# Kernel tuning notes

Hardware: AMD Instinct MI355X
Metric: run time of the kernel (lower is better)

The kernel has to match this reference:

```python
import jax, jax.numpy as jnp
import numpy as np

N_NODES = 50000
N_EDGES = 1600000
IN_DIM = 128
HID = 128
OUT_DIM = 3
NEG_SLOPE = 0.01  # LeakyReLU default


def _glorot(key, shape):
    fan_in, fan_out = shape[0], shape[1]
    lim = jnp.sqrt(6.0 / (fan_in + fan_out))
    return jax.random.uniform(key, shape, jnp.float32, -lim, lim)


def setup_inputs() -> dict:
    key = jax.random.key(0)
    ks = jax.random.split(key, 12)
    feature = jax.random.normal(ks[0], (N_NODES, IN_DIM), jnp.float32)
    edge_index = jax.random.randint(ks[1], (2, N_EDGES), 0, N_NODES, jnp.int64)
    edge_type = jax.random.randint(ks[2], (N_EDGES,), 0, 2, jnp.int64)
    return {
        'feature': feature,
        'edge_index': edge_index,
        'edge_type': edge_type,
        'W_in': _glorot(ks[3], (IN_DIM, HID)),
        'b_in': jnp.zeros((HID,), jnp.float32),
        'W1_l': _glorot(ks[4], (HID, HID)),  # SAGEConv lin_l (aggregated neighbors, has bias)
        'b1_l': jnp.zeros((HID,), jnp.float32),
        'W1_r': _glorot(ks[5], (HID, HID)),  # SAGEConv lin_r (root/self, no bias)
        'W2_l': _glorot(ks[6], (HID, HID)),
        'b2_l': jnp.zeros((HID,), jnp.float32),
        'W2_r': _glorot(ks[7], (HID, HID)),
        'W_out': _glorot(ks[8], (HID, OUT_DIM)),
        'b_out': jnp.zeros((OUT_DIM,), jnp.float32),
    }


def _sage_conv(x, src, dst, W_l, b_l, W_r):
    # PyG SAGEConv with mean aggregation: out = lin_l(mean_{j in N(i)} x_j) + lin_r(x_i)
    msg = x[src]                                              # [E, HID] gather
    summed = jax.ops.segment_sum(msg, dst, num_segments=x.shape[0])
    cnt = jax.ops.segment_sum(jnp.ones((src.shape[0],), x.dtype), dst,
                              num_segments=x.shape[0])
    agg = summed / jnp.maximum(cnt, 1.0)[:, None]             # isolated nodes -> 0
    return agg @ W_l + b_l + x @ W_r


def reference(feature, edge_index, edge_type, W_in, b_in, W1_l, b1_l, W1_r,
              W2_l, b2_l, W2_r, W_out, b_out):
    src, dst = edge_index[0], edge_index[1]
    x = jax.nn.leaky_relu(feature.astype(jnp.float32) @ W_in + b_in, NEG_SLOPE)
    x = _sage_conv(x, src, dst, W1_l, b1_l, W1_r)
    # dropout inactive in eval mode
    x = _sage_conv(x, src, dst, W2_l, b2_l, W2_r)
    return x @ W_out + b_out
```

## Files before the change

### kernel.cpp

```cpp
#include <hip/hip_runtime.h>
#include <hip/hip_bf16.h>

#define NEG_SLOPE 0.01f
#define BNODES 256
#define NBE 256

typedef __attribute__((ext_vector_type(8))) short short8;
typedef __attribute__((ext_vector_type(4))) float f32x4;
typedef __attribute__((ext_vector_type(2))) float f32x2;

__device__ __forceinline__ unsigned short f2bf(float f) {
  unsigned int u = __float_as_uint(f);
  u = (u + 0x7fffu + ((u >> 16) & 1u)) >> 16;
  return (unsigned short)u;
}
__device__ __forceinline__ float bf2f(unsigned short b) {
  return __uint_as_float(((unsigned)b) << 16);
}

#if defined(__has_builtin)
#if __has_builtin(__builtin_amdgcn_cvt_pk_f32_fp8) && __has_builtin(__builtin_amdgcn_cvt_pk_fp8_f32)
#define HAS_FP8_CVT 1
#endif
#endif
#ifndef HAS_FP8_CVT
#define HAS_FP8_CVT 0
#endif

__device__ __forceinline__ float dec1(unsigned b) {
  unsigned s = (b & 0x80u) << 24;
  unsigned em = b & 0x7fu;
  float v = (em < 8) ? (float)em * 0.001953125f
          : __uint_as_float((((em >> 3) + 120u) << 23) | ((em & 7u) << 20));
  return __uint_as_float(s ^ __float_as_uint(v));
}

__device__ __forceinline__ unsigned enc1(float f) {
  unsigned u = __float_as_uint(f);
  unsigned s = (u >> 24) & 0x80u;
  float a = fabsf(f);
  a = fminf(a, 480.f);
  unsigned code;
  if (a < 0.015625f) {
    code = (unsigned)__float2int_rn(a * 512.f);
  } else {
    unsigned ua = __float_as_uint(a);
    unsigned r = ua + 0x7ffffu + ((ua >> 20) & 1u);
    code = (((r >> 23) - 120u) << 3) | ((r >> 20) & 7u);
    if (code > 0x7fu) code = 0x7fu;
  }
  return s | code;
}

template<bool HI>
__device__ __forceinline__ f32x2 fp8pair(unsigned int w) {
#if HAS_FP8_CVT
  return __builtin_amdgcn_cvt_pk_f32_fp8((int)w, HI);
#else
  unsigned sh = HI ? 16u : 0u;
  f32x2 r;
  r[0] = dec1((w >> sh) & 0xffu);
  r[1] = dec1((w >> (sh + 8)) & 0xffu);
  return r;
#endif
}

template<bool HI>
__device__ __forceinline__ unsigned fp8pack(float a, float b, unsigned old) {
#if HAS_FP8_CVT
  return (unsigned)__builtin_amdgcn_cvt_pk_fp8_f32(a, b, (int)old, HI);
#else
  unsigned code = enc1(a) | (enc1(b) << 8);
  return HI ? ((old & 0x0000ffffu) | (code << 16)) : ((old & 0xffff0000u) | code);
#endif
}

__global__ __launch_bounds__(256) void k_prep_hist(
    const float* __restrict__ w0, const float* __restrict__ w1,
    const float* __restrict__ w2, const float* __restrict__ w3,
    const float* __restrict__ w4, unsigned short* __restrict__ wout,
    const int* __restrict__ dst, int* __restrict__ hist, int E)
{
  if (blockIdx.x < 5) {
    const float* srcs[5] = {w0, w1, w2, w3, w4};
    const float* s = srcs[blockIdx.x];
    unsigned short* o = wout + (size_t)blockIdx.x * 16384;
    for (int i = threadIdx.x; i < 16384; i += 256) {
      int c = i >> 7, k = i & 127;
      o[i] = f2bf(s[(size_t)k * 128 + c]);
    }
    return;
  }
  __shared__ int lh[256];
  const int bb = blockIdx.x - 5;
  int t = threadIdx.x;
  lh[t] = 0;
  __syncthreads();
  int chunk = (E + NBE - 1) / NBE;
  int s = bb * chunk;
  int e = min(E, s + chunk);
  for (int i = s + t; i < e; i += 256)
    atomicAdd(&lh[dst[i] >> 8], 1);
  __syncthreads();
  hist[bb * 256 + t] = lh[t];
}

__global__ __launch_bounds__(256) void k_scan(const int* __restrict__ hist,
    int* __restrict__ offs, int NB)
{
  __shared__ int tot[256];
  int t = threadIdx.x;
  int run = 0;
  #pragma unroll 8
  for (int b = 0; b < NBE; ++b) run += hist[b * 256 + t];
  tot[t] = run;
  __syncthreads();
  int val = run;
  for (int o = 1; o < 256; o <<= 1) {
    int x = (t >= o) ? tot[t - o] : 0;
    __syncthreads();
    val += x; tot[t] = val;
    __syncthreads();
  }
  int acc = val - run;
  #pragma unroll 8
  for (int b = 0; b < NBE; ++b) {
    offs[b * 256 + t] = acc;
    acc += hist[b * 256 + t];
  }
  (void)NB;
}

__global__ __launch_bounds__(256) void k_scatter(const int* __restrict__ src,
    const int* __restrict__ dst, const int* __restrict__ offs,
    unsigned int* __restrict__ recs, int E)
{
  __shared__ int lcnt[256];
  __shared__ int loff[256];
  int t = threadIdx.x;
  lcnt[t] = 0;
  loff[t] = offs[blockIdx.x * 256 + t];
  __syncthreads();
  int chunk = (E + NBE - 1) / NBE;
  int s = blockIdx.x * chunk;
  int e = min(E, s + chunk);
  for (int i = s + t; i < e; i += 256) {
    int d = dst[i];
    int b = d >> 8;
    int r = atomicAdd(&lcnt[b], 1);
    recs[loff[b] + r] = ((unsigned int)(d & 255) << 16) | (unsigned int)src[i];
  }
}

__device__ __forceinline__ void csr_body(int b, int* lcnt, int* lpos,
    const unsigned int* __restrict__ recs, const int* __restrict__ offs,
    int* __restrict__ adj, int* __restrict__ offs2, int* __restrict__ cnt,
    int N, int NB, int E)
{
  const int t  = threadIdx.x;
  const int bs = offs[b];
  const int be = (b + 1 < NB) ? offs[b + 1] : E;
  lcnt[t] = 0;
  __syncthreads();
  for (int i = bs + t; i < be; i += 256)
    atomicAdd(&lcnt[recs[i] >> 16], 1);
  __syncthreads();
  int v = lcnt[t];
  lpos[t] = v;
  __syncthreads();
  int val = v;
  for (int o = 1; o < 256; o <<= 1) {
    int x = (t >= o) ? lpos[t - o] : 0;
    __syncthreads();
    val += x; lpos[t] = val;
    __syncthreads();
  }
  int excl = val - v;
  int node = b * BNODES + t;
  if (node < N) { cnt[node] = v; offs2[node] = bs + excl; }
  lcnt[t] = excl;
  __syncthreads();
  for (int i = bs + t; i < be; i += 256) {
    unsigned int r = recs[i];
    int ld = r >> 16;
    int p = atomicAdd(&lcnt[ld], 1);
    adj[bs + p] = (int)(r & 0xffffu);
  }
}

template<bool ACT, bool HAS2, bool A1F32, bool EMIT8, bool OUTPROJ>
__device__ __forceinline__ void mgemm_body(int b, char* wlds,
    const void* __restrict__ A1v, const unsigned short* __restrict__ Wt1,
    const float* __restrict__ bias,
    const unsigned short* __restrict__ A2b, const unsigned short* __restrict__ Wt2,
    unsigned short* __restrict__ Cb, unsigned int* __restrict__ C8,
    const float* __restrict__ Wo, const float* __restrict__ bo,
    float* __restrict__ outp, int nrows)
{
  const int t    = threadIdx.x;
  const int wave = t >> 6;
  const int lane = t & 63;
  const int lr   = lane & 15;
  const int lg   = lane >> 4;
  const int r0   = b * 64 + wave * 16;
  int arow = r0 + lr; if (arow >= nrows) arow = nrows - 1;

  short8 a1[4], a2[4];
  #pragma unroll
  for (int ks = 0; ks < 4; ++ks) {
    const int k0 = ks * 32 + lg * 8;
    if (A1F32) {
      const float* A = (const float*)A1v;
      float4 f0 = *(const float4*)(A + (size_t)arow * 128 + k0);
      float4 f1 = *(const float4*)(A + (size_t)arow * 128 + k0 + 4);
      a1[ks][0] = (short)f2bf(f0.x); a1[ks][1] = (short)f2bf(f0.y);
      a1[ks][2] = (short)f2bf(f0.z); a1[ks][3] = (short)f2bf(f0.w);
      a1[ks][4] = (short)f2bf(f1.x); a1[ks][5] = (short)f2bf(f1.y);
      a1[ks][6] = (short)f2bf(f1.z); a1[ks][7] = (short)f2bf(f1.w);
    } else {
      a1[ks] = *(const short8*)((const unsigned short*)A1v + (size_t)arow * 128 + k0);
    }
  }
  if (HAS2) {
    #pragma unroll
    for (int ks = 0; ks < 4; ++ks) {
      const int k0 = ks * 32 + lg * 8;
      a2[ks] = *(const short8*)(A2b + (size_t)arow * 128 + k0);
    }
  }

  f32x4 acc[8];
  #pragma unroll
  for (int i = 0; i < 8; ++i) acc[i] = (f32x4){0.f, 0.f, 0.f, 0.f};

  #pragma unroll
  for (int i = 0; i < 8; ++i) {
    int o = (i * 256 + t) * 16;
    uint4 v = *(const uint4*)((const char*)Wt1 + o);
    int row = o >> 8, w = o & 255;
    *(uint4*)(wlds + row * 256 + (w ^ ((row & 7) << 4))) = v;
  }
  __syncthreads();
  #pragma unroll
  for (int ks = 0; ks < 4; ++ks) {
    #pragma unroll
    for (int cb = 0; cb < 8; ++cb) {
      int r = cb * 16 + lr;
      int wb = ks * 64 + lg * 16;
      short8 bv = *(const short8*)(wlds + r * 256 + (wb ^ ((r & 7) << 4)));
      acc[cb] = __builtin_amdgcn_mfma_f32_16x16x32_bf16(a1[ks], bv, acc[cb], 0, 0, 0);
    }
  }

  if (HAS2) {
    __syncthreads();
    #pragma unroll
    for (int i = 0; i < 8; ++i) {
      int o = (i * 256 + t) * 16;
      uint4 v = *(const uint4*)((const char*)Wt2 + o);
      int row = o >> 8, w = o & 255;
      *(uint4*)(wlds + row * 256 + (w ^ ((row & 7) << 4))) = v;
    }
    __syncthreads();
    #pragma unroll
    for (int ks = 0; ks < 4; ++ks) {
      #pragma unroll
      for (int cb = 0; cb < 8; ++cb) {
        int r = cb * 16 + lr;
        int wb = ks * 64 + lg * 16;
        short8 bv = *(const short8*)(wlds + r * 256 + (wb ^ ((r & 7) << 4)));
        acc[cb] = __builtin_amdgcn_mfma_f32_16x16x32_bf16(a2[ks], bv, acc[cb], 0, 0, 0);
      }
    }
  }

  __syncthreads();
  #pragma unroll
  for (int cb = 0; cb < 8; ++cb) {
    const int col = cb * 16 + lr;
    const float bcol = bias[col];
    #pragma unroll
    for (int reg = 0; reg < 4; ++reg) {
      const int lrow = wave * 16 + lg * 4 + reg;
      float o = acc[cb][reg] + bcol;
      if (ACT) o = o > 0.f ? o : o * NEG_SLOPE;
      *(unsigned short*)(wlds + lrow * 256 + col * 2) = f2bf(o);
    }
  }
  __syncthreads();

  if (!OUTPROJ) {
    #pragma unroll
    for (int i = 0; i < 4; ++i) {
      int idx = i * 256 + t;
      int row = idx >> 4, w = idx & 15;
      int r = b * 64 + row;
      if (r < nrows)
        *(uint4*)((char*)Cb + (size_t)r * 256 + w * 16) = *(const uint4*)(wlds + row * 256 + w * 16);
    }
    if (EMIT8) {
      #pragma unroll
      for (int i = 0; i < 4; ++i) {
        int idx = i * 256 + t;
        int row = idx >> 4, seg = idx & 15;
        int r = b * 64 + row;
        if (r < nrows) {
          const unsigned short* p = (const unsigned short*)(wlds + row * 256 + seg * 16);
          unsigned w0 = 0, w1 = 0;
          w0 = fp8pack<false>(bf2f(p[0]), bf2f(p[1]), w0);
          w0 = fp8pack<true >(bf2f(p[2]), bf2f(p[3]), w0);
          w1 = fp8pack<false>(bf2f(p[4]), bf2f(p[5]), w1);
          w1 = fp8pack<true >(bf2f(p[6]), bf2f(p[7]), w1);
          *(uint2*)(C8 + (size_t)r * 32 + seg * 2) = make_uint2(w0, w1);
        }
      }
    }
  } else {
    const int row = t >> 2, q = t & 3;
    const int r = b * 64 + row;
    float o0 = 0.f, o1 = 0.f, o2 = 0.f;
    const unsigned short* p = (const unsigned short*)(wlds + row * 256 + q * 64);
    #pragma unroll
    for (int i = 0; i < 32; ++i) {
      float x = bf2f(p[i]);
      const float* wr = Wo + (q * 32 + i) * 3;
      o0 += x * wr[0]; o1 += x * wr[1]; o2 += x * wr[2];
    }
    o0 += __shfl_xor(o0, 1, 64); o0 += __shfl_xor(o0, 2, 64);
    o1 += __shfl_xor(o1, 1, 64); o1 += __shfl_xor(o1, 2, 64);
    o2 += __shfl_xor(o2, 1, 64); o2 += __shfl_xor(o2, 2, 64);
    if (q == 0 && r < nrows) {
      outp[(size_t)r * 3 + 0] = o0 + bo[0];
      outp[(size_t)r * 3 + 1] = o1 + bo[1];
      outp[(size_t)r * 3 + 2] = o2 + bo[2];
    }
  }
}

__global__ __launch_bounds__(256) void k_csr_mgemm0(
    const unsigned int* __restrict__ recs, const int* __restrict__ offs,
    int* __restrict__ adj, int* __restrict__ offs2, int* __restrict__ cnt,
    const float* __restrict__ feature, const unsigned short* __restrict__ WtIn,
    const float* __restrict__ b_in,
    unsigned short* __restrict__ xbs, unsigned int* __restrict__ x8,
    int N, int NB, int E)
{
  __shared__ char wlds[32768];
  if ((int)blockIdx.x < NB) {
    int* li = (int*)wlds;
    csr_body(blockIdx.x, li, li + 256, recs, offs, adj, offs2, cnt, N, NB, E);
    return;
  }
  mgemm_body<true, false, true, true, false>(blockIdx.x - NB, wlds,
      feature, WtIn, b_in, nullptr, nullptr, xbs, x8, nullptr, nullptr, nullptr, N);
}

template<bool EMIT8, bool OUTPROJ>
__global__ __launch_bounds__(256) void k_mgemm(
    const unsigned short* __restrict__ A1b, const unsigned short* __restrict__ Wt1,
    const float* __restrict__ bias,
    const unsigned short* __restrict__ A2b, const unsigned short* __restrict__ Wt2,
    unsigned short* __restrict__ Cb, unsigned int* __restrict__ C8,
    const float* __restrict__ Wo, const float* __restrict__ bo,
    float* __restrict__ outp, int nrows)
{
  __shared__ char wlds[32768];
  mgemm_body<false, true, false, EMIT8, OUTPROJ>(blockIdx.x, wlds,
      A1b, Wt1, bias, A2b, Wt2, Cb, C8, Wo, bo, outp, nrows);
}

__global__ __launch_bounds__(256) void k_agg(const unsigned int* __restrict__ x8,
    const int* __restrict__ adj, const int* __restrict__ offs2,
    const int* __restrict__ cnt, unsigned int* __restrict__ aggb, int n, int nJ)
{
  const int Q   = (nJ + 7) >> 3;
  const int x   = blockIdx.x & 7;
  const int t2  = blockIdx.x >> 3;
  const int jj  = t2 % Q;
  const int sub = t2 / Q;
  const int j   = x + (jj << 3);
  if (j >= nJ) return;
  int node = j * 64 + sub * 4 + (threadIdx.x >> 6);
  if (node >= n) return;

  const int lane = threadIdx.x & 63;
  const int l = lane & 15;
  const int q = lane >> 4;
  const int c = cnt[node];
  const int* __restrict__ a = adj + offs2[node];

  f32x2 acc[4];
  #pragma unroll
  for (int jv = 0; jv < 4; ++jv) acc[jv] = (f32x2){0.f, 0.f};

  if (c > 0) {
    const int cm1 = c - 1;
    for (int e0 = 0; e0 < c; e0 += 32) {
      int idx[8];
      #pragma unroll
      for (int s = 0; s < 8; ++s)
        idx[s] = a[min(e0 + s * 4 + q, cm1)];
      uint2 v[8];
      #pragma unroll
      for (int s = 0; s < 8; ++s)
        v[s] = *(const uint2*)(x8 + (size_t)idx[s] * 32 + l * 2);
      #pragma unroll
      for (int s = 0; s < 8; ++s) {
        float m = (e0 + s * 4 + q < c) ? 1.f : 0.f;
        f32x2 mm = (f32x2){m, m};
        acc[0] += mm * fp8pair<false>(v[s].x);
        acc[1] += mm * fp8pair<true >(v[s].x);
        acc[2] += mm * fp8pair<false>(v[s].y);
        acc[3] += mm * fp8pair<true >(v[s].y);
      }
    }
    #pragma unroll
    for (int jv = 0; jv < 4; ++jv) {
      float a0 = acc[jv][0], a1 = acc[jv][1];
      a0 += __shfl_xor(a0, 16, 64);
      a0 += __shfl_xor(a0, 32, 64);
      a1 += __shfl_xor(a1, 16, 64);
      a1 += __shfl_xor(a1, 32, 64);
      acc[jv][0] = a0; acc[jv][1] = a1;
    }
  }

  if (q == 0) {
    float sc = (c > 0) ? 1.f / (float)c : 0.f;
    uint4 w;
    w.x = (unsigned)f2bf(acc[0][0] * sc) | ((unsigned)f2bf(acc[0][1] * sc) << 16);
    w.y = (unsigned)f2bf(acc[1][0] * sc) | ((unsigned)f2bf(acc[1][1] * sc) << 16);
    w.z = (unsigned)f2bf(acc[2][0] * sc) | ((unsigned)f2bf(acc[2][1] * sc) << 16);
    w.w = (unsigned)f2bf(acc[3][0] * sc) | ((unsigned)f2bf(acc[3][1] * sc) << 16);
    *(uint4*)(aggb + (size_t)node * 64 + l * 4) = w;
  }
}

extern "C" void kernel_launch(void* const* d_in, const int* in_sizes, int n_in,
                              void* d_out, int out_size, void* d_ws, size_t ws_size,
                              hipStream_t stream)
{
  const float* feature = (const float*)d_in[0];
  const int*   ei      = (const int*)d_in[1];
  const float* W_in = (const float*)d_in[3];
  const float* b_in = (const float*)d_in[4];
  const float* W1l  = (const float*)d_in[5];
  const float* b1l  = (const float*)d_in[6];
  const float* W1r  = (const float*)d_in[7];
  const float* W2l  = (const float*)d_in[8];
  const float* b2l  = (const float*)d_in[9];
  const float* W2r  = (const float*)d_in[10];
  const float* Wo   = (const float*)d_in[11];
  const float* bo   = (const float*)d_in[12];
  float* out = (float*)d_out;

  const int N = in_sizes[0] / 128;
  const int E = in_sizes[1] / 2;
  const int NB = (N + BNODES - 1) / BNODES;
  const int* src = ei;
  const int* dst = ei + E;

  char* ws = (char*)d_ws;
  size_t off = 0;
  auto alloc = [&](size_t bytes) {
    char* p = ws + off;
    off = (off + bytes + 255) & ~(size_t)255;
    return p;
  };
  unsigned int* xb    = (unsigned int*)alloc((size_t)N * 64 * 4);
  unsigned int* yb    = (unsigned int*)alloc((size_t)N * 64 * 4);
  unsigned int* agb   = (unsigned int*)alloc((size_t)N * 64 * 4);
  unsigned int* x8    = (unsigned int*)alloc((size_t)N * 32 * 4);
  unsigned int* y8    = (unsigned int*)alloc((size_t)N * 32 * 4);
  unsigned int* recs  = (unsigned int*)alloc((size_t)E * 4);
  int*          adj   = (int*)alloc((size_t)E * 4);
  int*          hist  = (int*)alloc((size_t)256 * NBE * 4);
  int*          offs  = (int*)alloc((size_t)256 * NBE * 4);
  int*          offs2 = (int*)alloc((size_t)N * 4);
  int*          cnt   = (int*)alloc((size_t)N * 4);
  unsigned short* wtb = (unsigned short*)alloc((size_t)5 * 16384 * 2);
  (void)ws_size; (void)n_in; (void)out_size;

  unsigned short* WtIn = wtb;
  unsigned short* Wt1l = wtb + 16384;
  unsigned short* Wt1r = wtb + 2 * 16384;
  unsigned short* Wt2l = wtb + 3 * 16384;
  unsigned short* Wt2r = wtb + 4 * 16384;

  unsigned short* xbs  = (unsigned short*)xb;
  unsigned short* ybs  = (unsigned short*)yb;
  unsigned short* agbs = (unsigned short*)agb;

  dim3 blk(256);
  int gGemm = (N + 63) / 64;
  int Q     = (gGemm + 7) / 8;
  int gAgg  = 8 * Q * 16;

  k_prep_hist<<<5 + NBE, blk, 0, stream>>>(W_in, W1l, W1r, W2l, W2r, wtb,
                                           dst, hist, E);
  k_scan<<<1, blk, 0, stream>>>(hist, offs, NB);
  k_scatter<<<NBE, blk, 0, stream>>>(src, dst, offs, recs, E);
  k_csr_mgemm0<<<NB + gGemm, blk, 0, stream>>>(recs, offs, adj, offs2, cnt,
      feature, WtIn, b_in, xbs, x8, N, NB, E);
  k_agg<<<gAgg, blk, 0, stream>>>(x8, adj, offs2, cnt, agb, N, gGemm);
  k_mgemm<true, false><<<gGemm, blk, 0, stream>>>(
      agbs, Wt1l, b1l, xbs, Wt1r, ybs, y8, nullptr, nullptr, nullptr, N);
  k_agg<<<gAgg, blk, 0, stream>>>(y8, adj, offs2, cnt, agb, N, gGemm);
  k_mgemm<false, true><<<gGemm, blk, 0, stream>>>(
      agbs, Wt2l, b2l, ybs, Wt2r, nullptr, nullptr, Wo, bo, out, N);
}
```

Measured before the change: 172.1 us.

## Fuse all pipeline stages into one cooperative persistent kernel with grid syncs

Replaces the eight separate kernel launches (prep/hist, scan, scatter, CSR+input GEMM, two aggregations, two GEMMs) with a single cooperative persistent kernel. The grid is sized from occupancy and uses grid.sync between stages, with blocks looping over virtual block IDs. The aim is to remove launch gaps and inter-kernel tail effects. In exchange, the grid is capped at 2048 blocks, the scan runs on one block while the rest wait, and the launch bounds hint of 4 blocks per unit may constrain registers. The old multi-launch path remains as a fallback if the cooperative launch fails.

Result: slower. 608.6 us (+253.7%).

```diff
diff --git a/kernel.cpp b/kernel.cpp
--- a/kernel.cpp
+++ b/kernel.cpp
@@ -1,5 +1,8 @@
 #include <hip/hip_runtime.h>
 #include <hip/hip_bf16.h>
+#include <hip/hip_cooperative_groups.h>
+
+namespace cg = cooperative_groups;
 
 #define NEG_SLOPE 0.01f
 #define BNODES 256
@@ -75,24 +78,23 @@
 #endif
 }
 
-__global__ __launch_bounds__(256) void k_prep_hist(
-    const float* __restrict__ w0, const float* __restrict__ w1,
-    const float* __restrict__ w2, const float* __restrict__ w3,
-    const float* __restrict__ w4, unsigned short* __restrict__ wout,
+
+__device__ __forceinline__ void prep_body(int vb,
+    const float* w0, const float* w1, const float* w2, const float* w3,
+    const float* w4, unsigned short* wout)
+{
+  const float* srcs[5] = {w0, w1, w2, w3, w4};
+  const float* s = srcs[vb];
+  unsigned short* o = wout + (size_t)vb * 16384;
+  for (int i = threadIdx.x; i < 16384; i += 256) {
+    int c = i >> 7, k = i & 127;
+    o[i] = f2bf(s[(size_t)k * 128 + c]);
+  }
+}
+
+__device__ __forceinline__ void hist_body(int bb, int* lh,
     const int* __restrict__ dst, int* __restrict__ hist, int E)
 {
-  if (blockIdx.x < 5) {
-    const float* srcs[5] = {w0, w1, w2, w3, w4};
-    const float* s = srcs[blockIdx.x];
-    unsigned short* o = wout + (size_t)blockIdx.x * 16384;
-    for (int i = threadIdx.x; i < 16384; i += 256) {
-      int c = i >> 7, k = i & 127;
-      o[i] = f2bf(s[(size_t)k * 128 + c]);
-    }
-    return;
-  }
-  __shared__ int lh[256];
-  const int bb = blockIdx.x - 5;
   int t = threadIdx.x;
   lh[t] = 0;
   __syncthreads();
@@ -105,10 +107,9 @@
   hist[bb * 256 + t] = lh[t];
 }
 
-__global__ __launch_bounds__(256) void k_scan(const int* __restrict__ hist,
-    int* __restrict__ offs, int NB)
-{
-  __shared__ int tot[256];
+__device__ __forceinline__ void scan_body(int* tot,
+    const int* __restrict__ hist, int* __restrict__ offs)
+{
   int t = threadIdx.x;
   int run = 0;
   #pragma unroll 8
@@ -128,21 +129,18 @@
     offs[b * 256 + t] = acc;
     acc += hist[b * 256 + t];
   }
-  (void)NB;
-}
-
-__global__ __launch_bounds__(256) void k_scatter(const int* __restrict__ src,
-    const int* __restrict__ dst, const int* __restrict__ offs,
-    unsigned int* __restrict__ recs, int E)
-{
-  __shared__ int lcnt[256];
-  __shared__ int loff[256];
+}
+
+__device__ __forceinline__ void scatter_body(int bb, int* lcnt, int* loff,
+    const int* __restrict__ src, const int* __restrict__ dst,
+    const int* __restrict__ offs, unsigned int* __restrict__ recs, int E)
+{
   int t = threadIdx.x;
   lcnt[t] = 0;
-  loff[t] = offs[blockIdx.x * 256 + t];
+  loff[t] = offs[bb * 256 + t];
   __syncthreads();
   int chunk = (E + NBE - 1) / NBE;
-  int s = blockIdx.x * chunk;
+  int s = bb * chunk;
   int e = min(E, s + chunk);
   for (int i = s + t; i < e; i += 256) {
     int d = dst[i];
@@ -337,45 +335,13 @@
   }
 }
 
-__global__ __launch_bounds__(256) void k_csr_mgemm0(
-    const unsigned int* __restrict__ recs, const int* __restrict__ offs,
-    int* __restrict__ adj, int* __restrict__ offs2, int* __restrict__ cnt,
-    const float* __restrict__ feature, const unsigned short* __restrict__ WtIn,
-    const float* __restrict__ b_in,
-    unsigned short* __restrict__ xbs, unsigned int* __restrict__ x8,
-    int N, int NB, int E)
-{
-  __shared__ char wlds[32768];
-  if ((int)blockIdx.x < NB) {
-    int* li = (int*)wlds;
-    csr_body(blockIdx.x, li, li + 256, recs, offs, adj, offs2, cnt, N, NB, E);
-    return;
-  }
-  mgemm_body<true, false, true, true, false>(blockIdx.x - NB, wlds,
-      feature, WtIn, b_in, nullptr, nullptr, xbs, x8, nullptr, nullptr, nullptr, N);
-}
-
-template<bool EMIT8, bool OUTPROJ>
-__global__ __launch_bounds__(256) void k_mgemm(
-    const unsigned short* __restrict__ A1b, const unsigned short* __restrict__ Wt1,
-    const float* __restrict__ bias,
-    const unsigned short* __restrict__ A2b, const unsigned short* __restrict__ Wt2,
-    unsigned short* __restrict__ Cb, unsigned int* __restrict__ C8,
-    const float* __restrict__ Wo, const float* __restrict__ bo,
-    float* __restrict__ outp, int nrows)
-{
-  __shared__ char wlds[32768];
-  mgemm_body<false, true, false, EMIT8, OUTPROJ>(blockIdx.x, wlds,
-      A1b, Wt1, bias, A2b, Wt2, Cb, C8, Wo, bo, outp, nrows);
-}
-
-__global__ __launch_bounds__(256) void k_agg(const unsigned int* __restrict__ x8,
+__device__ __forceinline__ void agg_body(int vb, const unsigned int* __restrict__ x8,
     const int* __restrict__ adj, const int* __restrict__ offs2,
     const int* __restrict__ cnt, unsigned int* __restrict__ aggb, int n, int nJ)
 {
   const int Q   = (nJ + 7) >> 3;
-  const int x   = blockIdx.x & 7;
-  const int t2  = blockIdx.x >> 3;
+  const int x   = vb & 7;
+  const int t2  = vb >> 3;
   const int jj  = t2 % Q;
   const int sub = t2 / Q;
   const int j   = x + (jj << 3);
@@ -436,6 +402,147 @@
   }
 }
 
+
+struct MegaArgs {
+  const float* feature;
+  const int* src; const int* dst;
+  const float *W_in, *b_in, *W1l, *b1l, *W1r, *W2l, *b2l, *W2r, *Wo, *bo;
+  unsigned short* wtb;
+  unsigned short* xbs; unsigned int* x8;
+  unsigned short* ybs; unsigned int* y8;
+  unsigned short* agbs; unsigned int* agb;
+  unsigned int* recs; int* adj; int* hist; int* offs; int* offs2; int* cnt;
+  float* out;
+  int N, E, NB, gGemm, gAgg;
+};
+
+__global__ __launch_bounds__(256, 4) void k_mega(MegaArgs a)
+{
+  __shared__ char smem[32768];
+  cg::grid_group grid = cg::this_grid();
+  const int G   = (int)gridDim.x;
+  const int bid = (int)blockIdx.x;
+
+  for (int vb = bid; vb < 5 + NBE; vb += G) {
+    if (vb < 5) prep_body(vb, a.W_in, a.W1l, a.W1r, a.W2l, a.W2r, a.wtb);
+    else        hist_body(vb - 5, (int*)smem, a.dst, a.hist, a.E);
+    __syncthreads();
+  }
+  grid.sync();
+
+  if (bid == 0) scan_body((int*)smem, a.hist, a.offs);
+  grid.sync();
+
+  for (int vb = bid; vb < NBE; vb += G) {
+    int* li = (int*)smem;
+    scatter_body(vb, li, li + 256, a.src, a.dst, a.offs, a.recs, a.E);
+    __syncthreads();
+  }
+  grid.sync();
+
+  for (int vb = bid; vb < a.NB + a.gGemm; vb += G) {
+    if (vb < a.NB) {
+      int* li = (int*)smem;
+      csr_body(vb, li, li + 256, a.recs, a.offs, a.adj, a.offs2, a.cnt, a.N, a.NB, a.E);
+    } else {
+      mgemm_body<true, false, true, true, false>(vb - a.NB, smem,
+          a.feature, a.wtb, a.b_in, nullptr, nullptr,
+          a.xbs, a.x8, nullptr, nullptr, nullptr, a.N);
+    }
+    __syncthreads();
+  }
+  grid.sync();
+
+  for (int vb = bid; vb < a.gAgg; vb += G)
+    agg_body(vb, a.x8, a.adj, a.offs2, a.cnt, a.agb, a.N, a.gGemm);
+  grid.sync();
+
+  for (int vb = bid; vb < a.gGemm; vb += G) {
+    mgemm_body<false, true, false, true, false>(vb, smem,
+        a.agbs, a.wtb + 16384, a.b1l, a.xbs, a.wtb + 2 * 16384,
+        a.ybs, a.y8, nullptr, nullptr, nullptr, a.N);
+    __syncthreads();
+  }
+  grid.sync();
+
+  for (int vb = bid; vb < a.gAgg; vb += G)
+    agg_body(vb, a.y8, a.adj, a.offs2, a.cnt, a.agb, a.N, a.gGemm);
+  grid.sync();
+
+  for (int vb = bid; vb < a.gGemm; vb += G) {
+    mgemm_body<false, true, false, false, true>(vb, smem,
+        a.agbs, a.wtb + 3 * 16384, a.b2l, a.ybs, a.wtb + 4 * 16384,
+        nullptr, nullptr, a.Wo, a.bo, a.out, a.N);
+    __syncthreads();
+  }
+}
+
+
+__global__ __launch_bounds__(256) void k_prep_hist(
+    const float* w0, const float* w1, const float* w2, const float* w3,
+    const float* w4, unsigned short* wout,
+    const int* __restrict__ dst, int* __restrict__ hist, int E)
+{
+  __shared__ int lh[256];
+  if (blockIdx.x < 5) { prep_body(blockIdx.x, w0, w1, w2, w3, w4, wout); return; }
+  hist_body(blockIdx.x - 5, lh, dst, hist, E);
+}
+
+__global__ __launch_bounds__(256) void k_scan(const int* __restrict__ hist,
+    int* __restrict__ offs)
+{
+  __shared__ int tot[256];
+  scan_body(tot, hist, offs);
+}
+
+__global__ __launch_bounds__(256) void k_scatter(const int* __restrict__ src,
+    const int* __restrict__ dst, const int* __restrict__ offs,
+    unsigned int* __restrict__ recs, int E)
+{
+  __shared__ int li[512];
+  scatter_body(blockIdx.x, li, li + 256, src, dst, offs, recs, E);
+}
+
+__global__ __launch_bounds__(256) void k_csr_mgemm0(
+    const unsigned int* __restrict__ recs, const int* __restrict__ offs,
+    int* __restrict__ adj, int* __restrict__ offs2, int* __restrict__ cnt,
+    const float* __restrict__ feature, const unsigned short* __restrict__ WtIn,
+    const float* __restrict__ b_in,
+    unsigned short* __restrict__ xbs, unsigned int* __restrict__ x8,
+    int N, int NB, int E)
+{
+  __shared__ char wlds[32768];
+  if ((int)blockIdx.x < NB) {
+    int* li = (int*)wlds;
+    csr_body(blockIdx.x, li, li + 256, recs, offs, adj, offs2, cnt, N, NB, E);
+    return;
+  }
+  mgemm_body<true, false, true, true, false>(blockIdx.x - NB, wlds,
+      feature, WtIn, b_in, nullptr, nullptr, xbs, x8, nullptr, nullptr, nullptr, N);
+}
+
+template<bool EMIT8, bool OUTPROJ>
+__global__ __launch_bounds__(256) void k_mgemm(
+    const unsigned short* __restrict__ A1b, const unsigned short* __restrict__ Wt1,
+    const float* __restrict__ bias,
+    const unsigned short* __restrict__ A2b, const unsigned short* __restrict__ Wt2,
+    unsigned short* __restrict__ Cb, unsigned int* __restrict__ C8,
+    const float* __restrict__ Wo, const float* __restrict__ bo,
+    float* __restrict__ outp, int nrows)
+{
+  __shared__ char wlds[32768];
+  mgemm_body<false, true, false, EMIT8, OUTPROJ>(blockIdx.x, wlds,
+      A1b, Wt1, bias, A2b, Wt2, Cb, C8, Wo, bo, outp, nrows);
+}
+
+__global__ __launch_bounds__(256) void k_agg(const unsigned int* __restrict__ x8,
+    const int* __restrict__ adj, const int* __restrict__ offs2,
+    const int* __restrict__ cnt, unsigned int* __restrict__ aggb, int n, int nJ)
+{
+  agg_body(blockIdx.x, x8, adj, offs2, cnt, aggb, n, nJ);
+}
+
+
 extern "C" void kernel_launch(void* const* d_in, const int* in_sizes, int n_in,
                               void* d_out, int out_size, void* d_ws, size_t ws_size,
                               hipStream_t stream)
@@ -481,31 +588,50 @@
   unsigned short* wtb = (unsigned short*)alloc((size_t)5 * 16384 * 2);
   (void)ws_size; (void)n_in; (void)out_size;
 
-  unsigned short* WtIn = wtb;
-  unsigned short* Wt1l = wtb + 16384;
-  unsigned short* Wt1r = wtb + 2 * 16384;
-  unsigned short* Wt2l = wtb + 3 * 16384;
-  unsigned short* Wt2r = wtb + 4 * 16384;
-
   unsigned short* xbs  = (unsigned short*)xb;
   unsigned short* ybs  = (unsigned short*)yb;
   unsigned short* agbs = (unsigned short*)agb;
 
-  dim3 blk(256);
   int gGemm = (N + 63) / 64;
   int Q     = (gGemm + 7) / 8;
   int gAgg  = 8 * Q * 16;
 
+  int bpc = 0;
+  hipError_t qrc = hipOccupancyMaxActiveBlocksPerMultiprocessor(&bpc, k_mega, 256, 0);
+  int G = (qrc == hipSuccess && bpc > 0) ? bpc * 256 : 1024;
+  if (G > 2048) G = 2048;
+  G &= ~7;
+  if (G < 8) G = 8;
+
+  MegaArgs a;
+  a.feature = feature; a.src = src; a.dst = dst;
+  a.W_in = W_in; a.b_in = b_in; a.W1l = W1l; a.b1l = b1l; a.W1r = W1r;
+  a.W2l = W2l; a.b2l = b2l; a.W2r = W2r; a.Wo = Wo; a.bo = bo;
+  a.wtb = wtb; a.xbs = xbs; a.x8 = x8; a.ybs = ybs; a.y8 = y8;
+  a.agbs = agbs; a.agb = agb;
+  a.recs = recs; a.adj = adj; a.hist = hist; a.offs = offs;
+  a.offs2 = offs2; a.cnt = cnt; a.out = out;
+  a.N = N; a.E = E; a.NB = NB; a.gGemm = gGemm; a.gAgg = gAgg;
+
+  void* kargs[] = { (void*)&a };
+  hipError_t rc = hipLaunchCooperativeKernel((const void*)k_mega, dim3(G), dim3(256),
+                                             kargs, 0, stream);
+  if (rc == hipSuccess) return;
+  (void)hipGetLastError();
+
+  dim3 blk(256);
   k_prep_hist<<<5 + NBE, blk, 0, stream>>>(W_in, W1l, W1r, W2l, W2r, wtb,
                                            dst, hist, E);
-  k_scan<<<1, blk, 0, stream>>>(hist, offs, NB);
+  k_scan<<<1, blk, 0, stream>>>(hist, offs);
   k_scatter<<<NBE, blk, 0, stream>>>(src, dst, offs, recs, E);
   k_csr_mgemm0<<<NB + gGemm, blk, 0, stream>>>(recs, offs, adj, offs2, cnt,
-      feature, WtIn, b_in, xbs, x8, N, NB, E);
+      feature, wtb, b_in, xbs, x8, N, NB, E);
   k_agg<<<gAgg, blk, 0, stream>>>(x8, adj, offs2, cnt, agb, N, gGemm);
   k_mgemm<true, false><<<gGemm, blk, 0, stream>>>(
-      agbs, Wt1l, b1l, xbs, Wt1r, ybs, y8, nullptr, nullptr, nullptr, N);
+      agbs, wtb + 16384, b1l, xbs, wtb + 2 * 16384, ybs, y8,
+      nullptr, nullptr, nullptr, N);
   k_agg<<<gAgg, blk, 0, stream>>>(y8, adj, offs2, cnt, agb, N, gGemm);
   k_mgemm<false, true><<<gGemm, blk, 0, stream>>>(
-      agbs, Wt2l, b2l, ybs, Wt2r, nullptr, nullptr, Wo, bo, out, N);
-}
+      agbs, wtb + 3 * 16384, b2l, ybs, wtb + 4 * 16384,
+      nullptr, nullptr, Wo, bo, out, N);
+}
```
